# Kernel tuning notes

Measured on AMD Instinct MI355X. Metric: run time of the kernel, lower is better.

Reference implementation:

```python
import jax, jax.numpy as jnp
import numpy as np

N, E = 100000, 1600000
F_IN, HID, C, L = 512, 128, 64, 64
ALPHA, THETA = 0.1, 0.5


def setup_inputs() -> dict:
    key = jax.random.key(0)
    ks = jax.random.split(key, 6)
    x = jax.random.normal(ks[0], (N, F_IN), jnp.float32)
    edge_index = jax.random.randint(ks[1], (2, E), 0, N, jnp.int32)
    W_in = jax.random.normal(ks[2], (F_IN, HID), jnp.float32) * (1.0 / np.sqrt(F_IN))
    b_in = jnp.zeros((HID,), jnp.float32)
    W_convs = jax.random.normal(ks[3], (L, HID, HID), jnp.float32) * (1.0 / np.sqrt(HID))
    W_out = jax.random.normal(ks[4], (HID, C), jnp.float32) * (1.0 / np.sqrt(HID))
    b_out = jnp.zeros((C,), jnp.float32)
    return {"x": x, "edge_index": edge_index, "W_in": W_in, "b_in": b_in,
            "W_convs": W_convs, "W_out": W_out, "b_out": b_out}


def reference(x, edge_index, W_in, b_in, W_convs, W_out, b_out):
    src, dst = edge_index[0], edge_index[1]
    # gcn_norm with self loops: A_hat = D^-1/2 (A + I) D^-1/2
    deg = jax.ops.segment_sum(jnp.ones((E,), x.dtype), dst, num_segments=N) + 1.0
    dinv = jax.lax.rsqrt(deg)
    ew = dinv[src] * dinv[dst]          # [E] off-diagonal weights
    self_w = dinv * dinv                # [N] self-loop weights

    def spmm(h):  # h: [N, HID]
        agg = jax.ops.segment_sum(h[src] * ew[:, None], dst, num_segments=N)
        return agg + self_w[:, None] * h

    # beta_l = log(theta / l + 1), l = 1..L
    betas = jnp.log(THETA / jnp.arange(1, L + 1, dtype=x.dtype) + 1.0)

    x0 = jax.nn.relu(x @ W_in + b_in)   # [N, HID]

    def layer(h, lw):
        W, beta = lw
        p = spmm(h)
        t = (1.0 - ALPHA) * p + ALPHA * x0          # initial residual
        out = (1.0 - beta) * t + beta * (t @ W)     # identity mapping (shared weights)
        return jax.nn.relu(out), None

    z, _ = jax.lax.scan(layer, x0, (W_convs, betas))
    logits = z @ W_out + b_out
    return z, jax.nn.log_softmax(logits, axis=-1)
```

## Files before the change

kernel.cpp:

```cpp
#include <hip/hip_runtime.h>
#include <hip/hip_bf16.h>

#define NN 100000
#define NE 1600000
#define F_IN 512
#define HID 128
#define C_OUT 64
#define L_LAYERS 64
#define SCAN_NB 98

using short8 = __attribute__((ext_vector_type(8))) short;
using f32x4  = __attribute__((ext_vector_type(4))) float;
typedef __attribute__((ext_vector_type(4))) unsigned short ushort4v;

__device__ __forceinline__ short f2bf(float f) {
    __hip_bfloat16 h = __float2bfloat16(f);
    return __builtin_bit_cast(short, h);
}
__device__ __forceinline__ unsigned short f2bfu(float f) {
    __hip_bfloat16 h = __float2bfloat16(f);
    return __builtin_bit_cast(unsigned short, h);
}
__device__ __forceinline__ float bflo(unsigned u) { return __uint_as_float(u << 16); }
__device__ __forceinline__ float bfhi(unsigned u) { return __uint_as_float(u & 0xffff0000u); }
__device__ __forceinline__ float bf2f(unsigned short u) { return __uint_as_float((unsigned)u << 16); }


__global__ void count_deg(const int* __restrict__ dst, int* __restrict__ cnt) {
    int e = blockIdx.x * blockDim.x + threadIdx.x;
    if (e < NE) atomicAdd(&cnt[dst[e]], 1);
}

__global__ void compute_dinv(const int* __restrict__ cnt, float* __restrict__ dinv) {
    int n = blockIdx.x * blockDim.x + threadIdx.x;
    if (n < NN) dinv[n] = rsqrtf((float)cnt[n] + 1.0f);
}

__global__ __launch_bounds__(256) void scan1(const int* __restrict__ cnt,
                                             int* __restrict__ row_ptr,
                                             int* __restrict__ partial) {
    __shared__ int sdata[256];
    int tid = threadIdx.x;
    int base = blockIdx.x * 1024;
    int v[4];
    int idx0 = base + tid * 4;
#pragma unroll
    for (int i = 0; i < 4; ++i) {
        int idx = idx0 + i;
        v[i] = (idx < NN) ? cnt[idx] : 0;
    }
    int s = v[0] + v[1] + v[2] + v[3];
    sdata[tid] = s;
    __syncthreads();
    int x = s;
    for (int off = 1; off < 256; off <<= 1) {
        int y = (tid >= off) ? sdata[tid - off] : 0;
        __syncthreads();
        x += y;
        sdata[tid] = x;
        __syncthreads();
    }
    int run = x - s;
#pragma unroll
    for (int i = 0; i < 4; ++i) {
        int idx = idx0 + i;
        if (idx < NN) row_ptr[idx] = run;
        run += v[i];
    }
    if (tid == 255) partial[blockIdx.x] = x;
}

__global__ __launch_bounds__(128) void scan2(int* __restrict__ partial) {
    __shared__ int sdata[128];
    int tid = threadIdx.x;
    int v = (tid < SCAN_NB) ? partial[tid] : 0;
    sdata[tid] = v;
    __syncthreads();
    int x = v;
    for (int off = 1; off < 128; off <<= 1) {
        int y = (tid >= off) ? sdata[tid - off] : 0;
        __syncthreads();
        x += y;
        sdata[tid] = x;
        __syncthreads();
    }
    if (tid < SCAN_NB) partial[tid] = x - v;
}

__global__ void scan3(int* __restrict__ row_ptr, const int* __restrict__ partial) {
    int idx = blockIdx.x * blockDim.x + threadIdx.x;
    if (idx < NN) row_ptr[idx] += partial[idx >> 10];
    else if (idx <= NN + 64) row_ptr[idx] = NE;
}

__global__ void scatter_csr(const int* __restrict__ src, const int* __restrict__ dst,
                            const float* __restrict__ dinv, int* __restrict__ fill,
                            int2* __restrict__ edges) {
    int e = blockIdx.x * blockDim.x + threadIdx.x;
    if (e >= NE) return;
    int s = src[e], d = dst[e];
    int pos = atomicAdd(&fill[d], 1);
    edges[pos] = make_int2(s, __float_as_int(dinv[s] * dinv[d]));
}

__global__ __launch_bounds__(256) void prep_wt(const float* __restrict__ Wc,
                                               const float* __restrict__ Win,
                                               __hip_bfloat16* __restrict__ WT,
                                               __hip_bfloat16* __restrict__ WinT) {
    int b = blockIdx.x, tid = threadIdx.x;
    if (b < 64) {
        const float* src = Wc + (size_t)b * HID * HID;
        __hip_bfloat16* dstp = WT + (size_t)b * HID * HID;
        for (int it = 0; it < 64; ++it) {
            int idx = it * 256 + tid;
            int n = idx >> 7, k = idx & 127;
            dstp[idx] = __float2bfloat16(src[k * HID + n]);
        }
    } else {
        int j = b - 64;
        for (int it = 0; it < 16; ++it) {
            int gid = j * 4096 + it * 256 + tid;
            int n = gid >> 9, k = gid & 511;
            WinT[gid] = __float2bfloat16(Win[k * HID + n]);
        }
    }
}

#define LOAD_SET(X0V, X1V, WVV, KT)                                              \
    {                                                                            \
        int k0_ = (KT) * 32;                                                     \
        _Pragma("unroll")                                                        \
        for (int i = 0; i < 2; ++i) {                                            \
            int id = i * 256 + tid;                                              \
            int rr = id >> 2, slot = id & 3;                                     \
            int grow = row0 + rr;                                                \
            X0V[i] = make_float4(0.f, 0.f, 0.f, 0.f); X1V[i] = X0V[i];           \
            if (grow < NN) {                                                     \
                X0V[i] = *(const float4*)&X[(size_t)grow * F_IN + k0_ + slot * 8];     \
                X1V[i] = *(const float4*)&X[(size_t)grow * F_IN + k0_ + slot * 8 + 4]; \
            }                                                                    \
            WVV[i] = *(const uint4*)&WinT[(size_t)rr * F_IN + k0_ + slot * 8];   \
        }                                                                        \
    }

#define PHASE(X0V, X1V, WVV, KT, BUF)                                            \
    {                                                                            \
        short* Xs = SMEM + (BUF) * 4096;                                         \
        short* Wsh = SMEM + 8192 + (BUF) * 4096;                                 \
        _Pragma("unroll")                                                        \
        for (int i = 0; i < 2; ++i) {                                            \
            int id = i * 256 + tid;                                              \
            int rr = id >> 2, slot = id & 3;                                     \
            short8 p;                                                            \
            p[0] = f2bf(X0V[i].x); p[1] = f2bf(X0V[i].y);                        \
            p[2] = f2bf(X0V[i].z); p[3] = f2bf(X0V[i].w);                        \
            p[4] = f2bf(X1V[i].x); p[5] = f2bf(X1V[i].y);                        \
            p[6] = f2bf(X1V[i].z); p[7] = f2bf(X1V[i].w);                        \
            *(short8*)&Xs[rr * 32 + (slot ^ ((rr >> 1) & 3)) * 8] = p;           \
            *(uint4*)&Wsh[rr * 32 + (slot ^ ((rr >> 1) & 3)) * 8] = WVV[i];      \
        }                                                                        \
        __syncthreads();                                                         \
        if ((KT) < 14) LOAD_SET(X0V, X1V, WVV, (KT) + 2);                        \
        short8 a[2], bb[8];                                                      \
        _Pragma("unroll")                                                        \
        for (int m = 0; m < 2; ++m) {                                            \
            int row = w * 32 + m * 16 + r;                                       \
            a[m] = *(short8*)&Xs[row * 32 + (g ^ ((row >> 1) & 3)) * 8];         \
        }                                                                        \
        _Pragma("unroll")                                                        \
        for (int n = 0; n < 8; ++n) {                                            \
            int row = n * 16 + r;                                                \
            bb[n] = *(short8*)&Wsh[row * 32 + (g ^ ((row >> 1) & 3)) * 8];       \
        }                                                                        \
        _Pragma("unroll")                                                        \
        for (int m = 0; m < 2; ++m)                                              \
            _Pragma("unroll")                                                    \
            for (int n = 0; n < 8; ++n)                                          \
                acc[m][n] = __builtin_amdgcn_mfma_f32_16x16x32_bf16(a[m], bb[n], acc[m][n], 0, 0, 0); \
    }

__global__ __launch_bounds__(256) void gemm_x0_mfma(const float* __restrict__ X,
                                                    const __hip_bfloat16* __restrict__ WinT,
                                                    const float* __restrict__ bias,
                                                    __hip_bfloat16* __restrict__ X0b) {
    __shared__ short SMEM[128 * 128];
    int tid = threadIdx.x;
    int w = tid >> 6, l = tid & 63, g = l >> 4, r = l & 15;
    int row0 = blockIdx.x * 128;
    f32x4 acc[2][8] = {};

    float4 ax0[2], ax1[2]; uint4 aw[2];
    float4 bx0[2], bx1[2]; uint4 bw[2];

    LOAD_SET(ax0, ax1, aw, 0);
    LOAD_SET(bx0, bx1, bw, 1);
    for (int kt = 0; kt < 16; kt += 2) {
        PHASE(ax0, ax1, aw, kt, 0);
        PHASE(bx0, bx1, bw, kt + 1, 1);
    }
    __syncthreads();
#pragma unroll
    for (int m = 0; m < 2; ++m) {
#pragma unroll
        for (int n = 0; n < 8; ++n) {
            int col = n * 16 + r;
            float bv = bias[col];
#pragma unroll
            for (int q = 0; q < 4; ++q) {
                int row = w * 32 + m * 16 + g * 4 + q;
                float v = fmaxf(acc[m][n][q] + bv, 0.f);
                SMEM[row * 128 + ((col >> 3) ^ (row & 15)) * 8 + (col & 7)] = f2bf(v);
            }
        }
    }
    __syncthreads();
#pragma unroll
    for (int i = 0; i < 8; ++i) {
        int id = i * 256 + tid;
        int rr = id >> 4, c8 = id & 15;
        int grow = row0 + rr;
        if (grow < NN)
            *(uint4*)&X0b[(size_t)grow * HID + c8 * 8] =
                *(uint4*)&SMEM[rr * 128 + ((c8 ^ (rr & 15)) * 8)];
    }
}

__global__ __launch_bounds__(512, 6) void layer_fused(const unsigned* __restrict__ H2,
                                                      const unsigned* __restrict__ X02,
                                                      const float* __restrict__ dinv,
                                                      const int* __restrict__ row_ptr,
                                                      const int2* __restrict__ edges,
                                                      const __hip_bfloat16* __restrict__ WTl,
                                                      float beta,
                                                      __hip_bfloat16* __restrict__ Hout,
                                                      float* __restrict__ Zf) {
    __shared__ short Ts[64 * 128];
    __shared__ short Ws[128 * 128];
    int tid = threadIdx.x;
    int w = tid >> 6, l = tid & 63, g = l >> 4, r = l & 15;
    int row0 = blockIdx.x * 64;

#pragma unroll
    for (int i = 0; i < 4; ++i) {
        int id = i * 512 + tid;
        int rr = id >> 4, slot = id & 15;
        uint4 wv = *(const uint4*)&WTl[(size_t)id * 8];
        *(uint4*)&Ws[rr * 128 + (slot ^ (rr & 15)) * 8] = wv;
    }

    unsigned* TsU = (unsigned*)Ts;
    int nb0 = row0 + w * 8;
    int ep[9];
#pragma unroll
    for (int k = 0; k < 9; ++k) ep[k] = __builtin_amdgcn_readfirstlane(row_ptr[nb0 + k]);

#pragma unroll
    for (int j = 0; j < 4; ++j) {
        int rrA = w * 8 + 2 * j, rrB = rrA + 1;
        int nA = row0 + rrA, nB = nA + 1;
        bool vA = nA < NN, vB = nB < NN;
        unsigned hsA = vA ? H2[((unsigned)nA << 6) + l] : 0u;
        unsigned hsB = vB ? H2[((unsigned)nB << 6) + l] : 0u;
        unsigned xvA = vA ? X02[((unsigned)nA << 6) + l] : 0u;
        unsigned xvB = vB ? X02[((unsigned)nB << 6) + l] : 0u;
        float dvA = vA ? dinv[nA] : 0.f, dvB = vB ? dinv[nB] : 0.f;
        float a0A = dvA * dvA * bflo(hsA), a1A = dvA * dvA * bfhi(hsA);
        float a0B = dvB * dvB * bflo(hsB), a1B = dvB * dvB * bfhi(hsB);
        int eA = ep[2 * j], e1A = ep[2 * j + 1];
        int eB = e1A, e1B = ep[2 * j + 2];
        while (eA < e1A || eB < e1B) {
            int cA = e1A - eA; cA = cA > 12 ? 12 : (cA < 0 ? 0 : cA);
            int cB = e1B - eB; cB = cB > 12 ? 12 : (cB < 0 ? 0 : cB);
            int sA[12], sB[12];
            float wA[12], wB[12];
#pragma unroll
            for (int u = 0; u < 12; ++u) {
                int2 t = edges[eA + u];
                sA[u] = (u < cA) ? t.x : 0;
                wA[u] = (u < cA) ? __int_as_float(t.y) : 0.f;
            }
#pragma unroll
            for (int u = 0; u < 12; ++u) {
                int2 t = edges[eB + u];
                sB[u] = (u < cB) ? t.x : 0;
                wB[u] = (u < cB) ? __int_as_float(t.y) : 0.f;
            }
            unsigned hvA[12], hvB[12];
#pragma unroll
            for (int u = 0; u < 12; ++u) hvA[u] = H2[((unsigned)sA[u] << 6) + l];
#pragma unroll
            for (int u = 0; u < 12; ++u) hvB[u] = H2[((unsigned)sB[u] << 6) + l];
#pragma unroll
            for (int u = 0; u < 12; ++u) {
                a0A = fmaf(wA[u], bflo(hvA[u]), a0A);
                a1A = fmaf(wA[u], bfhi(hvA[u]), a1A);
                a0B = fmaf(wB[u], bflo(hvB[u]), a0B);
                a1B = fmaf(wB[u], bfhi(hvB[u]), a1B);
            }
            eA += cA; eB += cB;
        }
        a0A = 0.9f * a0A + 0.1f * bflo(xvA);  a1A = 0.9f * a1A + 0.1f * bfhi(xvA);
        a0B = 0.9f * a0B + 0.1f * bflo(xvB);  a1B = 0.9f * a1B + 0.1f * bfhi(xvB);
        unsigned pkA = (unsigned)f2bfu(a0A) | ((unsigned)f2bfu(a1A) << 16);
        unsigned pkB = (unsigned)f2bfu(a0B) | ((unsigned)f2bfu(a1B) << 16);
        TsU[rrA * 64 + ((l >> 2) ^ (rrA & 15)) * 4 + (l & 3)] = pkA;
        TsU[rrB * 64 + ((l >> 2) ^ (rrB & 15)) * 4 + (l & 3)] = pkB;
    }
    __syncthreads();

    int nb = w & 3, cg = w >> 2;
    f32x4 acc[4] = {};
#pragma unroll
    for (int ks = 0; ks < 4; ++ks) {
        int rrT = nb * 16 + r;
        short8 bT = *(short8*)&Ts[rrT * 128 + ((ks * 4 + g) ^ (rrT & 15)) * 8];
        short8 aW[4];
#pragma unroll
        for (int c = 0; c < 4; ++c) {
            int rrW = (cg * 4 + c) * 16 + r;
            aW[c] = *(short8*)&Ws[rrW * 128 + ((ks * 4 + g) ^ (rrW & 15)) * 8];
        }
#pragma unroll
        for (int c = 0; c < 4; ++c)
            acc[c] = __builtin_amdgcn_mfma_f32_16x16x32_bf16(aW[c], bT, acc[c], 0, 0, 0);
    }

    float omb = 1.0f - beta;
    int node = nb * 16 + r;
    int grow = row0 + node;
    if (grow < NN) {
#pragma unroll
        for (int c = 0; c < 4; ++c) {
            int c0 = (cg * 4 + c) * 16 + g * 4;
            int slotE = c0 >> 3, posE = c0 & 7;
            ushort4v tv = *(ushort4v*)&Ts[node * 128 + (slotE ^ (node & 15)) * 8 + posE];
            float o[4];
#pragma unroll
            for (int q = 0; q < 4; ++q)
                o[q] = fmaxf(omb * bf2f(tv[q]) + beta * acc[c][q], 0.f);
            if (Zf) {
                *(float4*)&Zf[(size_t)grow * HID + c0] = make_float4(o[0], o[1], o[2], o[3]);
            } else {
                ushort4v hv;
#pragma unroll
                for (int q = 0; q < 4; ++q) hv[q] = f2bfu(o[q]);
                *(ushort4v*)&Hout[(size_t)grow * HID + c0] = hv;
            }
        }
    }
}

__global__ __launch_bounds__(256) void final_kernel(const float* __restrict__ Z,
                                                    const float* __restrict__ Wout,
                                                    const float* __restrict__ bout,
                                                    float* __restrict__ lo) {
    __shared__ float Wl[128 * 64];
    __shared__ float Zl[64][128];
    int tid = threadIdx.x;
    int w = tid >> 6, c = tid & 63;
    int n0 = blockIdx.x * 64;
#pragma unroll
    for (int i = 0; i < 8; ++i) {
        int id = i * 256 + tid;
        *(float4*)&Wl[id * 4] = *(const float4*)&Wout[(size_t)id * 4];
    }
#pragma unroll
    for (int i = 0; i < 8; ++i) {
        int id = i * 256 + tid;
        int rr = id >> 5, c4 = id & 31;
        int n = n0 + rr;
        float4 v = make_float4(0.f, 0.f, 0.f, 0.f);
        if (n < NN) v = *(const float4*)&Z[(size_t)n * HID + c4 * 4];
        *(float4*)&Zl[rr][c4 * 4] = v;
    }
    __syncthreads();
    float bv = bout[c];
#pragma unroll
    for (int i = 0; i < 4; ++i) {
        int nodeb = i * 16 + w * 4;
        float l0 = 0.f, l1 = 0.f, l2 = 0.f, l3 = 0.f;
#pragma unroll 8
        for (int k = 0; k < 128; ++k) {
            float wv = Wl[k * 64 + c];
            l0 = fmaf(Zl[nodeb + 0][k], wv, l0);
            l1 = fmaf(Zl[nodeb + 1][k], wv, l1);
            l2 = fmaf(Zl[nodeb + 2][k], wv, l2);
            l3 = fmaf(Zl[nodeb + 3][k], wv, l3);
        }
        float lg[4] = {l0 + bv, l1 + bv, l2 + bv, l3 + bv};
#pragma unroll
        for (int j = 0; j < 4; ++j) {
            float logit = lg[j];
            float m = logit;
#pragma unroll
            for (int off = 32; off; off >>= 1) m = fmaxf(m, __shfl_xor(m, off));
            float ex = __expf(logit - m);
            float ssum = ex;
#pragma unroll
            for (int off = 32; off; off >>= 1) ssum += __shfl_xor(ssum, off);
            int n = n0 + nodeb + j;
            if (n < NN) lo[(size_t)n * C_OUT + c] = logit - m - logf(ssum);
        }
    }
}

extern "C" void kernel_launch(void* const* d_in, const int* in_sizes, int n_in,
                              void* d_out, int out_size, void* d_ws, size_t ws_size,
                              hipStream_t stream) {
    const float* x = (const float*)d_in[0];
    const int* ei = (const int*)d_in[1];
    const int* src = ei;
    const int* dst = ei + NE;
    const float* W_in = (const float*)d_in[2];
    const float* b_in = (const float*)d_in[3];
    const float* W_convs = (const float*)d_in[4];
    const float* W_out = (const float*)d_in[5];
    const float* b_out = (const float*)d_in[6];
    float* out = (float*)d_out;

    char* ws = (char*)d_ws;
    float* dinv = (float*)ws;              ws += (size_t)NN * 4;
    int* row_ptr = (int*)ws;               ws += (size_t)(NN + 72) * 4;
    int* fill = (int*)ws;                  ws += (size_t)NN * 4;
    int* partial = (int*)ws;               ws += (size_t)128 * 4;
    int2* edges = (int2*)ws;               ws += (size_t)(NE + 32) * 8;
    __hip_bfloat16* WT = (__hip_bfloat16*)ws;   ws += (size_t)L_LAYERS * HID * HID * 2;
    __hip_bfloat16* WinT = (__hip_bfloat16*)ws; ws += (size_t)F_IN * HID * 2;
    __hip_bfloat16* x0b = (__hip_bfloat16*)ws;  ws += (size_t)NN * HID * 2;
    __hip_bfloat16* HbA = (__hip_bfloat16*)ws;  ws += (size_t)NN * HID * 2;
    __hip_bfloat16* HbB = (__hip_bfloat16*)ws;  ws += (size_t)NN * HID * 2;

    hipMemsetAsync(fill, 0, (size_t)NN * 4, stream);
    count_deg<<<(NE + 255) / 256, 256, 0, stream>>>(dst, fill);
    compute_dinv<<<(NN + 255) / 256, 256, 0, stream>>>(fill, dinv);
    scan1<<<SCAN_NB, 256, 0, stream>>>(fill, row_ptr, partial);
    scan2<<<1, 128, 0, stream>>>(partial);
    scan3<<<(NN + 255) / 256, 256, 0, stream>>>(row_ptr, partial);
    hipMemcpyAsync(fill, row_ptr, (size_t)NN * 4, hipMemcpyDeviceToDevice, stream);
    scatter_csr<<<(NE + 255) / 256, 256, 0, stream>>>(src, dst, dinv, fill, edges);
    prep_wt<<<80, 256, 0, stream>>>(W_convs, W_in, WT, WinT);

    int gemm_blocks = (NN + 127) / 128;
    gemm_x0_mfma<<<gemm_blocks, 256, 0, stream>>>(x, WinT, b_in, x0b);

    int layer_blocks = (NN + 63) / 64;
    float* zf = out;
    for (int l = 0; l < L_LAYERS; ++l) {
        const __hip_bfloat16* h_in = (l == 0) ? x0b : ((l & 1) ? HbA : HbB);
        __hip_bfloat16* h_out = (l & 1) ? HbB : HbA;
        float beta = logf(0.5f / (float)(l + 1) + 1.0f);
        bool last = (l == L_LAYERS - 1);
        layer_fused<<<layer_blocks, 512, 0, stream>>>(
            (const unsigned*)h_in, (const unsigned*)x0b, dinv, row_ptr, edges,
            WT + (size_t)l * HID * HID, beta,
            h_out, last ? zf : (float*)nullptr);
    }

    final_kernel<<<(NN + 63) / 64, 256, 0, stream>>>(zf, W_out, b_out, out + (size_t)NN * HID);
}
```

Measured before the change: 6.349 ms.

## Shrink input GEMM tile and add nontemporal loads/stores in layer kernel

The input projection GEMM moves from 128-row to 64-row tiles with a single-buffer register prefetch, smaller shared memory and twice as many blocks, aiming at better occupancy and tail balance. Separately, the per-layer fused kernel now uses nontemporal loads for the x0 residual and the CSR edge list, and nontemporal stores for the layer outputs, to keep the gathered H rows in cache. The risk is that nontemporal stores on H evict data the next layer re-reads, and the smaller GEMM tile reloads W more often.

```diff
diff --git a/kernel.cpp b/kernel.cpp
--- a/kernel.cpp
+++ b/kernel.cpp
@@ -11,6 +11,7 @@
 
 using short8 = __attribute__((ext_vector_type(8))) short;
 using f32x4  = __attribute__((ext_vector_type(4))) float;
+using u64    = unsigned long long;
 typedef __attribute__((ext_vector_type(4))) unsigned short ushort4v;
 
 __device__ __forceinline__ short f2bf(float f) {
@@ -24,6 +25,10 @@
 __device__ __forceinline__ float bflo(unsigned u) { return __uint_as_float(u << 16); }
 __device__ __forceinline__ float bfhi(unsigned u) { return __uint_as_float(u & 0xffff0000u); }
 __device__ __forceinline__ float bf2f(unsigned short u) { return __uint_as_float((unsigned)u << 16); }
+__device__ __forceinline__ int2 ld_nt_i2(const int2* p) {
+    u64 v = __builtin_nontemporal_load((const u64*)p);
+    return make_int2((int)(unsigned)v, (int)(unsigned)(v >> 32));
+}
 
 
 __global__ void count_deg(const int* __restrict__ dst, int* __restrict__ cnt) {
@@ -126,96 +131,83 @@
     }
 }
 
-#define LOAD_SET(X0V, X1V, WVV, KT)                                              \
-    {                                                                            \
-        int k0_ = (KT) * 32;                                                     \
-        _Pragma("unroll")                                                        \
-        for (int i = 0; i < 2; ++i) {                                            \
-            int id = i * 256 + tid;                                              \
-            int rr = id >> 2, slot = id & 3;                                     \
-            int grow = row0 + rr;                                                \
-            X0V[i] = make_float4(0.f, 0.f, 0.f, 0.f); X1V[i] = X0V[i];           \
-            if (grow < NN) {                                                     \
-                X0V[i] = *(const float4*)&X[(size_t)grow * F_IN + k0_ + slot * 8];     \
-                X1V[i] = *(const float4*)&X[(size_t)grow * F_IN + k0_ + slot * 8 + 4]; \
-            }                                                                    \
-            WVV[i] = *(const uint4*)&WinT[(size_t)rr * F_IN + k0_ + slot * 8];   \
-        }                                                                        \
-    }
-
-#define PHASE(X0V, X1V, WVV, KT, BUF)                                            \
-    {                                                                            \
-        short* Xs = SMEM + (BUF) * 4096;                                         \
-        short* Wsh = SMEM + 8192 + (BUF) * 4096;                                 \
-        _Pragma("unroll")                                                        \
-        for (int i = 0; i < 2; ++i) {                                            \
-            int id = i * 256 + tid;                                              \
-            int rr = id >> 2, slot = id & 3;                                     \
-            short8 p;                                                            \
-            p[0] = f2bf(X0V[i].x); p[1] = f2bf(X0V[i].y);                        \
-            p[2] = f2bf(X0V[i].z); p[3] = f2bf(X0V[i].w);                        \
-            p[4] = f2bf(X1V[i].x); p[5] = f2bf(X1V[i].y);                        \
-            p[6] = f2bf(X1V[i].z); p[7] = f2bf(X1V[i].w);                        \
-            *(short8*)&Xs[rr * 32 + (slot ^ ((rr >> 1) & 3)) * 8] = p;           \
-            *(uint4*)&Wsh[rr * 32 + (slot ^ ((rr >> 1) & 3)) * 8] = WVV[i];      \
-        }                                                                        \
-        __syncthreads();                                                         \
-        if ((KT) < 14) LOAD_SET(X0V, X1V, WVV, (KT) + 2);                        \
-        short8 a[2], bb[8];                                                      \
-        _Pragma("unroll")                                                        \
-        for (int m = 0; m < 2; ++m) {                                            \
-            int row = w * 32 + m * 16 + r;                                       \
-            a[m] = *(short8*)&Xs[row * 32 + (g ^ ((row >> 1) & 3)) * 8];         \
-        }                                                                        \
-        _Pragma("unroll")                                                        \
-        for (int n = 0; n < 8; ++n) {                                            \
-            int row = n * 16 + r;                                                \
-            bb[n] = *(short8*)&Wsh[row * 32 + (g ^ ((row >> 1) & 3)) * 8];       \
-        }                                                                        \
-        _Pragma("unroll")                                                        \
-        for (int m = 0; m < 2; ++m)                                              \
-            _Pragma("unroll")                                                    \
-            for (int n = 0; n < 8; ++n)                                          \
-                acc[m][n] = __builtin_amdgcn_mfma_f32_16x16x32_bf16(a[m], bb[n], acc[m][n], 0, 0, 0); \
-    }
-
 __global__ __launch_bounds__(256) void gemm_x0_mfma(const float* __restrict__ X,
                                                     const __hip_bfloat16* __restrict__ WinT,
                                                     const float* __restrict__ bias,
                                                     __hip_bfloat16* __restrict__ X0b) {
-    __shared__ short SMEM[128 * 128];
+    __shared__ short SMEM[12288];
     int tid = threadIdx.x;
     int w = tid >> 6, l = tid & 63, g = l >> 4, r = l & 15;
-    int row0 = blockIdx.x * 128;
-    f32x4 acc[2][8] = {};
-
-    float4 ax0[2], ax1[2]; uint4 aw[2];
-    float4 bx0[2], bx1[2]; uint4 bw[2];
-
-    LOAD_SET(ax0, ax1, aw, 0);
-    LOAD_SET(bx0, bx1, bw, 1);
-    for (int kt = 0; kt < 16; kt += 2) {
-        PHASE(ax0, ax1, aw, kt, 0);
-        PHASE(bx0, bx1, bw, kt + 1, 1);
-    }
-    __syncthreads();
-#pragma unroll
-    for (int m = 0; m < 2; ++m) {
+    int row0 = blockIdx.x * 64;
+    f32x4 acc[8] = {};
+
+    float4 sx0, sx1;
+    uint4 sw[2];
+    auto load_regs = [&](int kt) {
+        int k0 = kt * 32;
+        int rr = tid >> 2, slot = tid & 3;
+        int grow = row0 + rr;
+        sx0 = make_float4(0.f, 0.f, 0.f, 0.f); sx1 = sx0;
+        if (grow < NN) {
+            sx0 = *(const float4*)&X[(size_t)grow * F_IN + k0 + slot * 8];
+            sx1 = *(const float4*)&X[(size_t)grow * F_IN + k0 + slot * 8 + 4];
+        }
+#pragma unroll
+        for (int i = 0; i < 2; ++i) {
+            int id = i * 256 + tid;
+            int rw = id >> 2, slw = id & 3;
+            sw[i] = *(const uint4*)&WinT[(size_t)rw * F_IN + k0 + slw * 8];
+        }
+    };
+
+    load_regs(0);
+    for (int kt = 0; kt < 16; ++kt) {
+        short* Xs = SMEM + (kt & 1) * 6144;
+        short* Wsh = Xs + 2048;
+        {
+            int rr = tid >> 2, slot = tid & 3;
+            short8 p;
+            p[0] = f2bf(sx0.x); p[1] = f2bf(sx0.y); p[2] = f2bf(sx0.z); p[3] = f2bf(sx0.w);
+            p[4] = f2bf(sx1.x); p[5] = f2bf(sx1.y); p[6] = f2bf(sx1.z); p[7] = f2bf(sx1.w);
+            *(short8*)&Xs[rr * 32 + (slot ^ ((rr >> 1) & 3)) * 8] = p;
+#pragma unroll
+            for (int i = 0; i < 2; ++i) {
+                int id = i * 256 + tid;
+                int rw = id >> 2, slw = id & 3;
+                *(uint4*)&Wsh[rw * 32 + (slw ^ ((rw >> 1) & 3)) * 8] = sw[i];
+            }
+        }
+        __syncthreads();
+        if (kt < 15) load_regs(kt + 1);
+        short8 a, bb[8];
+        {
+            int row = w * 16 + r;
+            a = *(short8*)&Xs[row * 32 + (g ^ ((row >> 1) & 3)) * 8];
+        }
 #pragma unroll
         for (int n = 0; n < 8; ++n) {
-            int col = n * 16 + r;
-            float bv = bias[col];
-#pragma unroll
-            for (int q = 0; q < 4; ++q) {
-                int row = w * 32 + m * 16 + g * 4 + q;
-                float v = fmaxf(acc[m][n][q] + bv, 0.f);
-                SMEM[row * 128 + ((col >> 3) ^ (row & 15)) * 8 + (col & 7)] = f2bf(v);
-            }
-        }
-    }
-    __syncthreads();
-#pragma unroll
-    for (int i = 0; i < 8; ++i) {
+            int row = n * 16 + r;
+            bb[n] = *(short8*)&Wsh[row * 32 + (g ^ ((row >> 1) & 3)) * 8];
+        }
+#pragma unroll
+        for (int n = 0; n < 8; ++n)
+            acc[n] = __builtin_amdgcn_mfma_f32_16x16x32_bf16(a, bb[n], acc[n], 0, 0, 0);
+    }
+    __syncthreads();
+#pragma unroll
+    for (int n = 0; n < 8; ++n) {
+        int col = n * 16 + r;
+        float bv = bias[col];
+#pragma unroll
+        for (int q = 0; q < 4; ++q) {
+            int row = w * 16 + g * 4 + q;
+            float v = fmaxf(acc[n][q] + bv, 0.f);
+            SMEM[row * 128 + ((col >> 3) ^ (row & 15)) * 8 + (col & 7)] = f2bf(v);
+        }
+    }
+    __syncthreads();
+#pragma unroll
+    for (int i = 0; i < 4; ++i) {
         int id = i * 256 + tid;
         int rr = id >> 4, c8 = id & 15;
         int grow = row0 + rr;
@@ -261,8 +253,8 @@
         bool vA = nA < NN, vB = nB < NN;
         unsigned hsA = vA ? H2[((unsigned)nA << 6) + l] : 0u;
         unsigned hsB = vB ? H2[((unsigned)nB << 6) + l] : 0u;
-        unsigned xvA = vA ? X02[((unsigned)nA << 6) + l] : 0u;
-        unsigned xvB = vB ? X02[((unsigned)nB << 6) + l] : 0u;
+        unsigned xvA = vA ? __builtin_nontemporal_load(&X02[((unsigned)nA << 6) + l]) : 0u;
+        unsigned xvB = vB ? __builtin_nontemporal_load(&X02[((unsigned)nB << 6) + l]) : 0u;
         float dvA = vA ? dinv[nA] : 0.f, dvB = vB ? dinv[nB] : 0.f;
         float a0A = dvA * dvA * bflo(hsA), a1A = dvA * dvA * bfhi(hsA);
         float a0B = dvB * dvB * bflo(hsB), a1B = dvB * dvB * bfhi(hsB);
@@ -275,13 +267,13 @@
             float wA[12], wB[12];
 #pragma unroll
             for (int u = 0; u < 12; ++u) {
-                int2 t = edges[eA + u];
+                int2 t = ld_nt_i2(&edges[eA + u]);
                 sA[u] = (u < cA) ? t.x : 0;
                 wA[u] = (u < cA) ? __int_as_float(t.y) : 0.f;
             }
 #pragma unroll
             for (int u = 0; u < 12; ++u) {
-                int2 t = edges[eB + u];
+                int2 t = ld_nt_i2(&edges[eB + u]);
                 sB[u] = (u < cB) ? t.x : 0;
                 wB[u] = (u < cB) ? __int_as_float(t.y) : 0.f;
             }
@@ -339,12 +331,13 @@
             for (int q = 0; q < 4; ++q)
                 o[q] = fmaxf(omb * bf2f(tv[q]) + beta * acc[c][q], 0.f);
             if (Zf) {
-                *(float4*)&Zf[(size_t)grow * HID + c0] = make_float4(o[0], o[1], o[2], o[3]);
+                f32x4 ov = {o[0], o[1], o[2], o[3]};
+                __builtin_nontemporal_store(ov, (f32x4*)&Zf[(size_t)grow * HID + c0]);
             } else {
                 ushort4v hv;
 #pragma unroll
                 for (int q = 0; q < 4; ++q) hv[q] = f2bfu(o[q]);
-                *(ushort4v*)&Hout[(size_t)grow * HID + c0] = hv;
+                __builtin_nontemporal_store(hv, (ushort4v*)&Hout[(size_t)grow * HID + c0]);
             }
         }
     }
@@ -440,7 +433,7 @@
     scatter_csr<<<(NE + 255) / 256, 256, 0, stream>>>(src, dst, dinv, fill, edges);
     prep_wt<<<80, 256, 0, stream>>>(W_convs, W_in, WT, WinT);
 
-    int gemm_blocks = (NN + 127) / 128;
+    int gemm_blocks = (NN + 63) / 64;
     gemm_x0_mfma<<<gemm_blocks, 256, 0, stream>>>(x, WinT, b_in, x0b);
 
     int layer_blocks = (NN + 63) / 64;
```

New measurement: 6.812 ms. 1.07x slower.
